# Optimization experiments

Measured on AMD Instinct MI355X. Metric: run time of the kernel, lower is better.

Reference implementation:

```python
import jax, jax.numpy as jnp
import numpy as np

N_NODES = 100000
N_EDGES = 1600000
D_FEAT = 128


def setup_inputs() -> dict:
    key = jax.random.key(0)
    k1, k2, k3, k4 = jax.random.split(key, 4)
    support = jax.random.normal(k1, (N_NODES, D_FEAT), dtype=jnp.float32)
    vals = jax.random.uniform(k2, (N_EDGES,), dtype=jnp.float32)
    rows = jax.random.randint(k3, (N_EDGES,), 0, N_NODES, dtype=jnp.int64)
    cols = jax.random.randint(k4, (N_EDGES,), 0, N_NODES, dtype=jnp.int64)
    return {"support": support, "vals": vals, "rows": rows, "cols": cols}


def reference(support, vals, rows, cols):
    # out = adj @ support, adj given in COO: adj[rows[e], cols[e]] = vals[e]
    # Gather neighbor features, scale by edge weight, scatter-add to row nodes.
    msgs = vals[:, None] * support[cols]          # [E, F]
    out = jax.ops.segment_sum(msgs, rows, num_segments=support.shape[0])  # [N, F]
    return out
```

## Files before the change

kernel.cpp:

```cpp
#include <hip/hip_runtime.h>
#include <hip/hip_bf16.h>
#include <hip/hip_fp16.h>


#define D_FEAT 128
#define F4 32
#define H4 32
#define H8 16
#define STRIDE 64
#define CELL 32
#define OVF_CAP 131072
#define EPT 8
#define MAXIT 8
#define MAXSLOT 8192

typedef float    vfloat4 __attribute__((ext_vector_type(4)));
typedef _Float16 half4v  __attribute__((ext_vector_type(4)));
typedef _Float16 half8v  __attribute__((ext_vector_type(8)));


__global__ __launch_bounds__(1024) void
bin_kernel(const int* __restrict__ rows,
           const int* __restrict__ cols,
           const float* __restrict__ vals,
           int2* __restrict__ coarse,
           int* __restrict__ cellcnt,
           int4* __restrict__ ovf,
           int* __restrict__ ovf_count,
           int E, int BT, int NBLK, int ND) {
    int b = blockIdx.x;
    int tid = threadIdx.x;

    __shared__ int hist[512];
    for (int i = tid; i < 512; i += 1024) hist[i] = 0;
    __syncthreads();

    int t = b * 1024 + tid;
    int   r[EPT];
    int   c[EPT];
    float v[EPT];
    int   rk[EPT];

    #pragma unroll
    for (int i = 0; i < EPT; ++i) {
        int e = t + i * BT;
        r[i] = (e < E) ? rows[e] : -1;
    }
    #pragma unroll
    for (int i = 0; i < EPT; ++i) {
        int e = t + i * BT;
        if (e < E) { c[i] = cols[e]; v[i] = vals[e]; }
    }
    #pragma unroll
    for (int i = 0; i < EPT; ++i)
        rk[i] = (r[i] >= 0) ? atomicAdd(&hist[r[i] >> 8], 1) : 0;

    #pragma unroll
    for (int i = 0; i < EPT; ++i) {
        if (r[i] < 0) continue;
        int d = r[i] >> 8;
        if (rk[i] < CELL) {
            int2 q;
            q.x = ((r[i] & 255) << 17) | c[i];
            q.y = __float_as_int(v[i]);
            coarse[((size_t)d * NBLK + b) * CELL + rk[i]] = q;
        } else {
            int o = atomicAdd(ovf_count, 1);
            if (o < OVF_CAP) {
                int4 q;
                q.x = r[i]; q.y = c[i]; q.z = __float_as_int(v[i]); q.w = 0;
                ovf[o] = q;
            }
        }
    }
    __syncthreads();
    for (int d = tid; d < ND; d += 1024) {
        int h = hist[d];
        cellcnt[(size_t)d * NBLK + b] = (h < CELL) ? h : CELL;
    }
}


__global__ void convert_kernel(const float4* __restrict__ in,
                               half8v* __restrict__ out, int n8) {
    int t = blockIdx.x * blockDim.x + threadIdx.x;
    if (t >= n8) return;
    float4 a = in[(size_t)t * 2];
    float4 b = in[(size_t)t * 2 + 1];
    half8v h;
    h[0] = (_Float16)a.x; h[1] = (_Float16)a.y;
    h[2] = (_Float16)a.z; h[3] = (_Float16)a.w;
    h[4] = (_Float16)b.x; h[5] = (_Float16)b.y;
    h[6] = (_Float16)b.z; h[7] = (_Float16)b.w;
    out[t] = h;
}


__global__ __launch_bounds__(1024) void
bucket_csr_gather_kernel(const half8v* __restrict__ supporth,
                         const int2* __restrict__ coarse,
                         const int* __restrict__ cellcnt,
                         float4* __restrict__ out4,
                         int NBLK, int N) {
    __shared__ int  cnt[257];
    __shared__ int  off[257];
    __shared__ int2 csr[MAXSLOT + 8];

    const int d   = blockIdx.x;
    const int tid = threadIdx.x;
    const int2* cbase = coarse  + (size_t)d * NBLK * CELL;
    const int*  ccnt  = cellcnt + (size_t)d * NBLK;
    const int total = NBLK * CELL;

    if (tid < 257) cnt[tid] = 0;
    __syncthreads();

    int2 ent[MAXIT];
    int  err[MAXIT];
    int  ernk[MAXIT];
    #pragma unroll
    for (int it = 0; it < MAXIT; ++it) {
        int s = tid + it * 1024;
        err[it] = -1;
        if (s < total && (s & (CELL - 1)) < ccnt[s >> 5]) {
            int2 q = cbase[s];
            int r = (q.x >> 17) & 255;
            ent[it].x = q.x & 0x1FFFF;
            ent[it].y = q.y;
            err[it] = r;
            ernk[it] = atomicAdd(&cnt[r], 1);
        }
    }
    __syncthreads();

    if (tid < 64) {
        int4 c4 = ((int4*)cnt)[tid];
        int t0 = c4.x;
        int t1 = t0 + c4.y;
        int t2 = t1 + c4.z;
        int t3 = t2 + c4.w;
        int inc = t3;
        #pragma unroll
        for (int dd = 1; dd < 64; dd <<= 1) {
            int t = __shfl_up(inc, dd, 64);
            if (tid >= dd) inc += t;
        }
        int excl = inc - t3;
        off[tid * 4 + 0] = excl;
        off[tid * 4 + 1] = excl + t0;
        off[tid * 4 + 2] = excl + t1;
        off[tid * 4 + 3] = excl + t2;
        if (tid == 63) off[256] = inc;
    }
    __syncthreads();

    #pragma unroll
    for (int it = 0; it < MAXIT; ++it) {
        if (err[it] >= 0)
            csr[off[err[it]] + ernk[it]] = ent[it];
    }
    __syncthreads();

    const int g = tid >> 4;
    const int i = tid & 15;
    const int base = d << 8;
    for (int rq = 0; rq < 4; ++rq) {
        int r   = (rq << 6) + g;
        int beg = off[r];
        int end = off[r + 1];
        vfloat4 a00 = {0.f,0.f,0.f,0.f}, a01 = {0.f,0.f,0.f,0.f};
        vfloat4 a10 = {0.f,0.f,0.f,0.f}, a11 = {0.f,0.f,0.f,0.f};
        for (int k0 = beg; k0 < end; k0 += 8) {
            int   cc[8];
            float vv[8];
            #pragma unroll
            for (int u = 0; u < 8; ++u) {
                int2 e = csr[k0 + u];
                bool ib = (k0 + u) < end;
                cc[u] = ib ? e.x : 0;
                vv[u] = ib ? __int_as_float(e.y) : 0.f;
            }
            half8v s[8];
            #pragma unroll
            for (int u = 0; u < 8; ++u)
                s[u] = supporth[(size_t)cc[u] * H8 + i];
            #pragma unroll
            for (int u = 0; u < 8; ++u) {
                float v = vv[u];
                if (u & 1) {
                    a10.x += v * (float)s[u][0];
                    a10.y += v * (float)s[u][1];
                    a10.z += v * (float)s[u][2];
                    a10.w += v * (float)s[u][3];
                    a11.x += v * (float)s[u][4];
                    a11.y += v * (float)s[u][5];
                    a11.z += v * (float)s[u][6];
                    a11.w += v * (float)s[u][7];
                } else {
                    a00.x += v * (float)s[u][0];
                    a00.y += v * (float)s[u][1];
                    a00.z += v * (float)s[u][2];
                    a00.w += v * (float)s[u][3];
                    a01.x += v * (float)s[u][4];
                    a01.y += v * (float)s[u][5];
                    a01.z += v * (float)s[u][6];
                    a01.w += v * (float)s[u][7];
                }
            }
        }
        int row = base + r;
        if (row < N) {
            vfloat4 r0, r1;
            r0.x = a00.x + a10.x; r0.y = a00.y + a10.y;
            r0.z = a00.z + a10.z; r0.w = a00.w + a10.w;
            r1.x = a01.x + a11.x; r1.y = a01.y + a11.y;
            r1.z = a01.z + a11.z; r1.w = a01.w + a11.w;
            float4* dst = &out4[(size_t)row * F4 + (i << 1)];
            __builtin_nontemporal_store(r0, (vfloat4*)dst);
            __builtin_nontemporal_store(r1, (vfloat4*)(dst + 1));
        }
    }
}


__global__ void ovf_scatter_kernel(const float* __restrict__ support,
                                   const int4* __restrict__ ovf,
                                   const int* __restrict__ ovf_count,
                                   float* __restrict__ out, int cap) {
    int gid = blockIdx.x * blockDim.x + threadIdx.x;
    int i = gid >> 5;
    int j = gid & 31;
    int istride = (gridDim.x * blockDim.x) >> 5;
    int cnt = *ovf_count;
    if (cnt > cap) cnt = cap;
    for (; i < cnt; i += istride) {
        int4 q = ovf[i];
        float v = __int_as_float(q.z);
        const float4* s4 = (const float4*)support + (size_t)q.y * F4 + j;
        float4 s = *s4;
        float* o = out + (size_t)q.x * D_FEAT + j * 4;
        unsafeAtomicAdd(o + 0, v * s.x);
        unsafeAtomicAdd(o + 1, v * s.y);
        unsafeAtomicAdd(o + 2, v * s.z);
        unsafeAtomicAdd(o + 3, v * s.w);
    }
}


__global__ void gather_half_kernel(const half4v* __restrict__ supporth,
                                   const int* __restrict__ cursor,
                                   const int2* __restrict__ pairs,
                                   float4* __restrict__ out4, int n_nodes) {
    unsigned int t = blockIdx.x * blockDim.x + threadIdx.x;
    unsigned int row = t >> 5;
    unsigned int j = t & 31;
    if (row >= (unsigned int)n_nodes) return;
    int deg = cursor[row];
    if (deg > STRIDE) deg = STRIDE;
    const int2* pr = pairs + (size_t)row * STRIDE;
    int2 z = {0, 0};
    int2 p0 = ((int)j < deg) ? pr[j] : z;
    int2 p1 = ((int)(j + 32) < deg) ? pr[j + 32] : z;
    int   c0 = p0.x;  float v0 = __int_as_float(p0.y);
    int   c1 = p1.x;  float v1 = __int_as_float(p1.y);
    int degr = (deg + 7) & ~7;
    float4 acc[4];
    #pragma unroll
    for (int u = 0; u < 4; ++u) acc[u] = {0.f, 0.f, 0.f, 0.f};
    for (int k = 0; k < degr; k += 8) {
        int   cc[8];
        float vv[8];
        #pragma unroll
        for (int u = 0; u < 8; ++u) {
            int kk = k + u;
            cc[u] = __shfl(kk < 32 ? c0 : c1, kk & 31, 32);
            vv[u] = __shfl(kk < 32 ? v0 : v1, kk & 31, 32);
        }
        half4v s[8];
        #pragma unroll
        for (int u = 0; u < 8; ++u)
            s[u] = supporth[(size_t)cc[u] * H4 + j];
        #pragma unroll
        for (int u = 0; u < 8; ++u) {
            acc[u & 3].x += vv[u] * (float)s[u][0];
            acc[u & 3].y += vv[u] * (float)s[u][1];
            acc[u & 3].z += vv[u] * (float)s[u][2];
            acc[u & 3].w += vv[u] * (float)s[u][3];
        }
    }
    vfloat4 res;
    res.x = (acc[0].x + acc[1].x) + (acc[2].x + acc[3].x);
    res.y = (acc[0].y + acc[1].y) + (acc[2].y + acc[3].y);
    res.z = (acc[0].z + acc[1].z) + (acc[2].z + acc[3].z);
    res.w = (acc[0].w + acc[1].w) + (acc[2].w + acc[3].w);
    __builtin_nontemporal_store(res, (vfloat4*)&out4[(size_t)row * F4 + j]);
}

__global__ void bucket_ilp_kernel(const int* __restrict__ rows,
                                  const int* __restrict__ cols,
                                  const float* __restrict__ vals,
                                  int* __restrict__ cursor,
                                  int* __restrict__ ovf_count,
                                  int2* __restrict__ pairs,
                                  int4* __restrict__ ovf,
                                  int n_edges, int gstride) {
    int tid = blockIdx.x * blockDim.x + threadIdx.x;
    int   r[EPT];
    int   c[EPT];
    float v[EPT];
    int   slot[EPT];
    #pragma unroll
    for (int i = 0; i < EPT; ++i) {
        int e = tid + i * gstride;
        r[i] = (e < n_edges) ? rows[e] : -1;
    }
    #pragma unroll
    for (int i = 0; i < EPT; ++i) {
        int e = tid + i * gstride;
        if (e < n_edges) { c[i] = cols[e]; v[i] = vals[e]; }
    }
    #pragma unroll
    for (int i = 0; i < EPT; ++i)
        slot[i] = (r[i] >= 0) ? atomicAdd(&cursor[r[i]], 1) : 0;
    #pragma unroll
    for (int i = 0; i < EPT; ++i) {
        if (r[i] < 0) continue;
        int2 p;
        p.x = c[i];
        p.y = __float_as_int(v[i]);
        if (slot[i] < STRIDE) {
            pairs[(size_t)r[i] * STRIDE + slot[i]] = p;
        } else {
            int o = atomicAdd(ovf_count, 1);
            if (o < OVF_CAP) {
                int4 q; q.x = r[i]; q.y = p.x; q.z = p.y; q.w = 0;
                ovf[o] = q;
            }
        }
    }
}


__global__ void gc_scatter_kernel(const float* __restrict__ support,
                                  const float* __restrict__ vals,
                                  const int* __restrict__ rows,
                                  const int* __restrict__ cols,
                                  float* __restrict__ out, int n_edges) {
    unsigned int t = blockIdx.x * blockDim.x + threadIdx.x;
    unsigned int e = t >> 5;
    unsigned int j = t & 31;
    if (e >= (unsigned int)n_edges) return;
    int r = rows[e];
    int c = cols[e];
    float v = vals[e];
    const float4* s4 = reinterpret_cast<const float4*>(support) + (size_t)c * F4 + j;
    float4 s = *s4;
    float* o = out + (size_t)r * D_FEAT + j * 4;
    unsafeAtomicAdd(o + 0, v * s.x);
    unsafeAtomicAdd(o + 1, v * s.y);
    unsafeAtomicAdd(o + 2, v * s.z);
    unsafeAtomicAdd(o + 3, v * s.w);
}


extern "C" void kernel_launch(void* const* d_in, const int* in_sizes, int n_in,
                              void* d_out, int out_size, void* d_ws, size_t ws_size,
                              hipStream_t stream) {
    const float* support = (const float*)d_in[0];
    const float* vals    = (const float*)d_in[1];
    const int*   rows    = (const int*)d_in[2];
    const int*   cols    = (const int*)d_in[3];
    float* out = (float*)d_out;

    int E = in_sizes[1];
    int N = in_sizes[0] / D_FEAT;
    int n8 = N * D_FEAT / 8;
    int ND = (N + 255) >> 8;
    int NBLK = (E + 1024 * EPT - 1) / (1024 * EPT);
    int BT = NBLK * 1024;

    char* ws = (char*)d_ws;
    size_t cur = 0;
    auto carve = [&](size_t bytes) -> void* {
        void* p = ws + cur;
        cur += (bytes + 255) & ~(size_t)255;
        return p;
    };

    {
        size_t save = cur;
        int2*   coarse    = (int2*)carve((size_t)ND * NBLK * CELL * 8);
        int*    cellcnt   = (int*)carve((size_t)ND * NBLK * 4);
        int4*   ovf       = (int4*)carve((size_t)OVF_CAP * 16);
        int*    ovf_count = (int*)carve(256);
        half8v* supporth  = (half8v*)carve((size_t)N * D_FEAT * 2);
        if (cur <= ws_size && ND <= 512 && NBLK * CELL <= MAXSLOT) {
            (void)hipMemsetAsync(ovf_count, 0, 4, stream);
            bin_kernel<<<NBLK, 1024, 0, stream>>>(
                rows, cols, vals, coarse, cellcnt, ovf, ovf_count,
                E, BT, NBLK, ND);
            convert_kernel<<<(n8 + 255) / 256, 256, 0, stream>>>(
                (const float4*)support, supporth, n8);
            bucket_csr_gather_kernel<<<ND, 1024, 0, stream>>>(
                supporth, coarse, cellcnt, (float4*)out, NBLK, N);
            ovf_scatter_kernel<<<512, 256, 0, stream>>>(
                support, ovf, ovf_count, out, OVF_CAP);
            return;
        }
        cur = save;
    }

    {
        size_t save = cur;
        int*    cursor   = (int*)carve((size_t)(N + 1) * 4);
        int2*   pairs    = (int2*)carve((size_t)N * STRIDE * 8);
        int4*   ovf      = (int4*)carve((size_t)8192 * 16);
        half8v* supporth = (half8v*)carve((size_t)N * D_FEAT * 2);
        if (cur <= ws_size) {
            int* ovf_count = cursor + N;
            int bthreads = (E + EPT - 1) / EPT;
            int bblocks = (bthreads + 255) / 256;
            int gstride = bblocks * 256;
            (void)hipMemsetAsync(cursor, 0, (size_t)(N + 1) * 4, stream);
            convert_kernel<<<(n8 + 255) / 256, 256, 0, stream>>>(
                (const float4*)support, supporth, n8);
            bucket_ilp_kernel<<<bblocks, 256, 0, stream>>>(
                rows, cols, vals, cursor, ovf_count, pairs, ovf, E, gstride);
            unsigned int gthreads = (unsigned int)N * 32;
            gather_half_kernel<<<(gthreads + 255) / 256, 256, 0, stream>>>(
                (const half4v*)supporth, cursor, pairs, (float4*)out, N);
            ovf_scatter_kernel<<<512, 256, 0, stream>>>(
                support, ovf, ovf_count, out, 8192);
            return;
        }
        cur = save;
    }

    (void)hipMemsetAsync(d_out, 0, (size_t)out_size * sizeof(float), stream);
    unsigned int total = (unsigned int)E * 32;
    gc_scatter_kernel<<<(total + 255) / 256, 256, 0, stream>>>(
        support, vals, rows, cols, out, E);
}
```

Measured before the change: 211.2 us.

## Halve bucket size to 128 rows and fuse fp16 convert into bin kernel

Each bucket now covers 128 rows instead of 256, with cells of 16 instead of 32. The gather runs 782 blocks of 512 threads and uses a much smaller shared CSR buffer, which should raise occupancy and spread the gather across more CUs. The fp32-to-fp16 conversion of support moves into extra blocks of the binning kernel, removing one launch and letting conversion overlap with binning. The cost is more edges spilling past the smaller cells into the atomic overflow path, and a bigger histogram in the binning kernel.

```diff
diff --git a/kernel.cpp b/kernel.cpp
--- a/kernel.cpp
+++ b/kernel.cpp
@@ -8,11 +8,12 @@
 #define H4 32
 #define H8 16
 #define STRIDE 64
-#define CELL 32
+#define CELL 16
 #define OVF_CAP 131072
 #define EPT 8
-#define MAXIT 8
-#define MAXSLOT 8192
+#define MAXIT 7
+#define MAXSLOT 3136
+#define BROWS 128
 
 typedef float    vfloat4 __attribute__((ext_vector_type(4)));
 typedef _Float16 half4v  __attribute__((ext_vector_type(4)));
@@ -20,19 +21,36 @@
 
 
 __global__ __launch_bounds__(1024) void
-bin_kernel(const int* __restrict__ rows,
-           const int* __restrict__ cols,
-           const float* __restrict__ vals,
-           int2* __restrict__ coarse,
-           int* __restrict__ cellcnt,
-           int4* __restrict__ ovf,
-           int* __restrict__ ovf_count,
-           int E, int BT, int NBLK, int ND) {
+phase1_bin_kernel(const float4* __restrict__ support4,
+                  half8v* __restrict__ supporth,
+                  const int* __restrict__ rows,
+                  const int* __restrict__ cols,
+                  const float* __restrict__ vals,
+                  int2* __restrict__ coarse,
+                  int* __restrict__ cellcnt,
+                  int4* __restrict__ ovf,
+                  int* __restrict__ ovf_count,
+                  int E, int BT, int NBLK, int ND, int n8) {
     int b = blockIdx.x;
     int tid = threadIdx.x;
 
-    __shared__ int hist[512];
-    for (int i = tid; i < 512; i += 1024) hist[i] = 0;
+    if (b >= NBLK) {
+        int m = (b - NBLK) * 1024 + tid;
+        if (m < n8) {
+            float4 a0 = support4[(size_t)m * 2];
+            float4 a1 = support4[(size_t)m * 2 + 1];
+            half8v h;
+            h[0] = (_Float16)a0.x; h[1] = (_Float16)a0.y;
+            h[2] = (_Float16)a0.z; h[3] = (_Float16)a0.w;
+            h[4] = (_Float16)a1.x; h[5] = (_Float16)a1.y;
+            h[6] = (_Float16)a1.z; h[7] = (_Float16)a1.w;
+            supporth[m] = h;
+        }
+        return;
+    }
+
+    __shared__ int hist[1024];
+    for (int i = tid; i < 1024; i += 1024) hist[i] = 0;
     __syncthreads();
 
     int t = b * 1024 + tid;
@@ -53,15 +71,15 @@
     }
     #pragma unroll
     for (int i = 0; i < EPT; ++i)
-        rk[i] = (r[i] >= 0) ? atomicAdd(&hist[r[i] >> 8], 1) : 0;
+        rk[i] = (r[i] >= 0) ? atomicAdd(&hist[r[i] >> 7], 1) : 0;
 
     #pragma unroll
     for (int i = 0; i < EPT; ++i) {
         if (r[i] < 0) continue;
-        int d = r[i] >> 8;
+        int d = r[i] >> 7;
         if (rk[i] < CELL) {
             int2 q;
-            q.x = ((r[i] & 255) << 17) | c[i];
+            q.x = ((r[i] & 127) << 17) | c[i];
             q.y = __float_as_int(v[i]);
             coarse[((size_t)d * NBLK + b) * CELL + rk[i]] = q;
         } else {
@@ -81,29 +99,14 @@
 }
 
 
-__global__ void convert_kernel(const float4* __restrict__ in,
-                               half8v* __restrict__ out, int n8) {
-    int t = blockIdx.x * blockDim.x + threadIdx.x;
-    if (t >= n8) return;
-    float4 a = in[(size_t)t * 2];
-    float4 b = in[(size_t)t * 2 + 1];
-    half8v h;
-    h[0] = (_Float16)a.x; h[1] = (_Float16)a.y;
-    h[2] = (_Float16)a.z; h[3] = (_Float16)a.w;
-    h[4] = (_Float16)b.x; h[5] = (_Float16)b.y;
-    h[6] = (_Float16)b.z; h[7] = (_Float16)b.w;
-    out[t] = h;
-}
-
-
-__global__ __launch_bounds__(1024) void
+__global__ __launch_bounds__(512) void
 bucket_csr_gather_kernel(const half8v* __restrict__ supporth,
                          const int2* __restrict__ coarse,
                          const int* __restrict__ cellcnt,
                          float4* __restrict__ out4,
                          int NBLK, int N) {
-    __shared__ int  cnt[257];
-    __shared__ int  off[257];
+    __shared__ int  cnt[BROWS + 1];
+    __shared__ int  off[BROWS + 1];
     __shared__ int2 csr[MAXSLOT + 8];
 
     const int d   = blockIdx.x;
@@ -112,7 +115,7 @@
     const int*  ccnt  = cellcnt + (size_t)d * NBLK;
     const int total = NBLK * CELL;
 
-    if (tid < 257) cnt[tid] = 0;
+    if (tid < BROWS + 1) cnt[tid] = 0;
     __syncthreads();
 
     int2 ent[MAXIT];
@@ -120,11 +123,11 @@
     int  ernk[MAXIT];
     #pragma unroll
     for (int it = 0; it < MAXIT; ++it) {
-        int s = tid + it * 1024;
+        int s = tid + it * 512;
         err[it] = -1;
-        if (s < total && (s & (CELL - 1)) < ccnt[s >> 5]) {
+        if (s < total && (s & (CELL - 1)) < ccnt[s >> 4]) {
             int2 q = cbase[s];
-            int r = (q.x >> 17) & 255;
+            int r = (q.x >> 17) & 127;
             ent[it].x = q.x & 0x1FFFF;
             ent[it].y = q.y;
             err[it] = r;
@@ -133,7 +136,7 @@
     }
     __syncthreads();
 
-    if (tid < 64) {
+    if (tid < 32) {
         int4 c4 = ((int4*)cnt)[tid];
         int t0 = c4.x;
         int t1 = t0 + c4.y;
@@ -141,8 +144,8 @@
         int t3 = t2 + c4.w;
         int inc = t3;
         #pragma unroll
-        for (int dd = 1; dd < 64; dd <<= 1) {
-            int t = __shfl_up(inc, dd, 64);
+        for (int dd = 1; dd < 32; dd <<= 1) {
+            int t = __shfl_up(inc, dd, 32);
             if (tid >= dd) inc += t;
         }
         int excl = inc - t3;
@@ -150,7 +153,7 @@
         off[tid * 4 + 1] = excl + t0;
         off[tid * 4 + 2] = excl + t1;
         off[tid * 4 + 3] = excl + t2;
-        if (tid == 63) off[256] = inc;
+        if (tid == 31) off[BROWS] = inc;
     }
     __syncthreads();
 
@@ -163,9 +166,9 @@
 
     const int g = tid >> 4;
     const int i = tid & 15;
-    const int base = d << 8;
+    const int base = d << 7;
     for (int rq = 0; rq < 4; ++rq) {
-        int r   = (rq << 6) + g;
+        int r   = (rq << 5) + g;
         int beg = off[r];
         int end = off[r + 1];
         vfloat4 a00 = {0.f,0.f,0.f,0.f}, a01 = {0.f,0.f,0.f,0.f};
@@ -247,6 +250,20 @@
 }
 
 
+__global__ void convert_kernel(const float4* __restrict__ in,
+                               half8v* __restrict__ out, int n8) {
+    int t = blockIdx.x * blockDim.x + threadIdx.x;
+    if (t >= n8) return;
+    float4 a = in[(size_t)t * 2];
+    float4 b = in[(size_t)t * 2 + 1];
+    half8v h;
+    h[0] = (_Float16)a.x; h[1] = (_Float16)a.y;
+    h[2] = (_Float16)a.z; h[3] = (_Float16)a.w;
+    h[4] = (_Float16)b.x; h[5] = (_Float16)b.y;
+    h[6] = (_Float16)b.z; h[7] = (_Float16)b.w;
+    out[t] = h;
+}
+
 __global__ void gather_half_kernel(const half4v* __restrict__ supporth,
                                    const int* __restrict__ cursor,
                                    const int2* __restrict__ pairs,
@@ -375,7 +392,7 @@
     int E = in_sizes[1];
     int N = in_sizes[0] / D_FEAT;
     int n8 = N * D_FEAT / 8;
-    int ND = (N + 255) >> 8;
+    int ND = (N + BROWS - 1) / BROWS;
     int NBLK = (E + 1024 * EPT - 1) / (1024 * EPT);
     int BT = NBLK * 1024;
 
@@ -394,14 +411,13 @@
         int4*   ovf       = (int4*)carve((size_t)OVF_CAP * 16);
         int*    ovf_count = (int*)carve(256);
         half8v* supporth  = (half8v*)carve((size_t)N * D_FEAT * 2);
-        if (cur <= ws_size && ND <= 512 && NBLK * CELL <= MAXSLOT) {
+        if (cur <= ws_size && ND <= 1024 && NBLK * CELL <= MAXSLOT) {
             (void)hipMemsetAsync(ovf_count, 0, 4, stream);
-            bin_kernel<<<NBLK, 1024, 0, stream>>>(
-                rows, cols, vals, coarse, cellcnt, ovf, ovf_count,
-                E, BT, NBLK, ND);
-            convert_kernel<<<(n8 + 255) / 256, 256, 0, stream>>>(
-                (const float4*)support, supporth, n8);
-            bucket_csr_gather_kernel<<<ND, 1024, 0, stream>>>(
+            int cblocks = (n8 + 1023) / 1024;
+            phase1_bin_kernel<<<NBLK + cblocks, 1024, 0, stream>>>(
+                (const float4*)support, supporth, rows, cols, vals,
+                coarse, cellcnt, ovf, ovf_count, E, BT, NBLK, ND, n8);
+            bucket_csr_gather_kernel<<<ND, 512, 0, stream>>>(
                 supporth, coarse, cellcnt, (float4*)out, NBLK, N);
             ovf_scatter_kernel<<<512, 256, 0, stream>>>(
                 support, ovf, ovf_count, out, OVF_CAP);
```

After: 265.8 us. 25.9% more time.
